# Performance work log

Measured on AMD Instinct MI355X. Metric: run time of the kernel, lower is better.

Reference implementation:

```python
import jax, jax.numpy as jnp
import numpy as np

N_NODES = 100000
N_EDGES = 1000000
IN_DIM = 64
HID = 64
OUT_DIM = 32
NUM_GRAPHS = 512


def setup_inputs() -> dict:
    key = jax.random.key(0)
    ks = jax.random.split(key, 16)
    x = jax.random.normal(ks[0], (N_NODES, IN_DIM), dtype=jnp.float32)
    edge_index = jax.random.randint(ks[1], (2, N_EDGES), 0, N_NODES, dtype=jnp.int64)
    batch = jnp.sort(jax.random.randint(ks[2], (N_NODES,), 0, NUM_GRAPHS, dtype=jnp.int64))

    def lin(k, i, o):
        s = 1.0 / np.sqrt(i)
        kw, kb = jax.random.split(k)
        return (jax.random.uniform(kw, (i, o), jnp.float32, -s, s),
                jax.random.uniform(kb, (o,), jnp.float32, -s, s))

    W1a, b1a = lin(ks[3], IN_DIM, HID)
    W2a, b2a = lin(ks[4], HID, HID)
    W1b, b1b = lin(ks[5], HID, HID)
    W2b, b2b = lin(ks[6], HID, HID)
    Wp1, bp1 = lin(ks[7], HID, HID)
    Wp2, bp2 = lin(ks[8], HID, OUT_DIM)
    return dict(x=x, edge_index=edge_index, batch=batch,
                W1a=W1a, b1a=b1a, W2a=W2a, b2a=b2a,
                W1b=W1b, b1b=b1b, W2b=W2b, b2b=b2b,
                Wp1=Wp1, bp1=bp1, Wp2=Wp2, bp2=bp2)


def _gin_layer(x, edge_index, W1, b1, W2, b2):
    # GINConv (eps=0): h_i = MLP(x_i + sum_{j->i} x_j)
    src, dst = edge_index[0], edge_index[1]
    agg = jax.ops.segment_sum(x[src], dst, num_segments=N_NODES)  # [N, d]
    h = x + agg
    h = jnp.maximum(h @ W1 + b1, 0.0) @ W2 + b2
    return h


def reference(x, edge_index, batch,
              W1a, b1a, W2a, b2a,
              W1b, b1b, W2b, b2b,
              Wp1, bp1, Wp2, bp2):
    # layer 0 (dropout is identity in eval mode)
    x = _gin_layer(x, edge_index, W1a, b1a, W2a, b2a)
    x = jnp.maximum(x, 0.0)
    # layer 1
    x = _gin_layer(x, edge_index, W1b, b1b, W2b, b2b)
    emb = x  # pre-ReLU embedding of last executed conv
    x = jnp.maximum(x, 0.0)
    # global mean pool over graphs
    sums = jax.ops.segment_sum(x, batch, num_segments=NUM_GRAPHS)  # [G, d]
    cnts = jax.ops.segment_sum(jnp.ones((x.shape[0],), x.dtype), batch, num_segments=NUM_GRAPHS)
    pooled = sums / jnp.maximum(cnts, 1.0)[:, None]
    # post-MLP (dropout identity in eval)
    out = (pooled @ Wp1 + bp1) @ Wp2 + bp2
    return emb, jax.nn.log_softmax(out, axis=1)
```

## Files before the change

kernel.cpp:

```cpp
#include <hip/hip_runtime.h>
#include <math.h>

#define N_NODES 100000
#define N_EDGES 1000000
#define HID 64
#define OUT_DIM 32
#define NUM_GRAPHS 512
#define CAP 48
#define NBUCK 98
#define BCAP 11264
#define ACHUNK 4096

typedef __attribute__((ext_vector_type(4))) float f4v;
typedef __attribute__((ext_vector_type(4))) int i4v;
typedef __attribute__((ext_vector_type(8))) short s8v;

static __device__ inline short f2bf(float f) {
  unsigned u = __float_as_uint(f);
  unsigned r = (u + 0x7fffu + ((u >> 16) & 1u)) >> 16;
  return (short)r;
}
static __device__ inline float bf2f(short s) {
  return __uint_as_float(((unsigned)(unsigned short)s) << 16);
}

__global__ __launch_bounds__(256) void prep_kernel(
    const float* __restrict__ W1a, const float* __restrict__ W2a,
    const float* __restrict__ W1b, const float* __restrict__ W2b,
    short* __restrict__ wtab, const int* __restrict__ batch,
    int* __restrict__ starts, int* __restrict__ bcnt) {
  int t = blockIdx.x * 256 + threadIdx.x;
  if (t < 16384) {
    int which = t >> 12;
    int r = t & 4095;
    const float* W = (which == 0) ? W1a : (which == 1) ? W2a : (which == 2) ? W1b : W2b;
    short* hiT = wtab + which * 8192;
    short* loT = hiT + 4096;
    int n = r & 63, k = r >> 6;
    float w = W[k * HID + n];
    short h = f2bf(w);
    hiT[n * HID + k] = h;
    loT[n * HID + k] = f2bf(w - bf2f(h));
  } else if (t < 16384 + NUM_GRAPHS + 1) {
    int g = t - 16384;
    int lo = 0, hi = N_NODES;
    while (lo < hi) {
      int mid = (lo + hi) >> 1;
      if (batch[mid] < g) lo = mid + 1; else hi = mid;
    }
    starts[g] = lo;
  } else if (t < 16384 + NUM_GRAPHS + 1 + NBUCK) {
    bcnt[t - 16384 - NUM_GRAPHS - 1] = 0;
  }
}

__global__ __launch_bounds__(256) void bucket_kernel(
    const int* __restrict__ ei, int* __restrict__ bedge,
    int* __restrict__ bcnt, int n_edges) {
  __shared__ int s_pack[ACHUNK];
  __shared__ unsigned char s_b[ACHUNK];
  __shared__ int s_sorted[ACHUNK];
  __shared__ int s_hist[NBUCK];
  __shared__ int s_off[NBUCK];
  __shared__ int s_base[NBUCK];

  int e0 = blockIdx.x * ACHUNK;
  int n = n_edges - e0;
  if (n > ACHUNK) n = ACHUNK;

  for (int i = threadIdx.x; i < NBUCK; i += 256) s_hist[i] = 0;
  __syncthreads();

  for (int i = threadIdx.x; i < n; i += 256) {
    int src = ei[e0 + i];
    int dst = ei[n_edges + e0 + i];
    int b = dst >> 10;
    s_pack[i] = src | ((dst & 1023) << 17);
    s_b[i] = (unsigned char)b;
    atomicAdd(&s_hist[b], 1);
  }
  __syncthreads();

  if (threadIdx.x == 0) {
    int run = 0;
    for (int b = 0; b < NBUCK; b++) { s_off[b] = run; run += s_hist[b]; }
  }
  if (threadIdx.x < NBUCK) {
    int c = s_hist[threadIdx.x];
    s_base[threadIdx.x] = c > 0 ? atomicAdd(&bcnt[threadIdx.x], c) : 0;
  }
  __syncthreads();

  for (int i = threadIdx.x; i < n; i += 256) {
    int p = atomicAdd(&s_off[s_b[i]], 1);
    s_sorted[p] = s_pack[i];
  }
  __syncthreads();

  int wv = threadIdx.x >> 6;
  int lane = threadIdx.x & 63;
  for (int b = wv; b < NBUCK; b += 4) {
    int cnt = s_hist[b];
    if (cnt == 0) continue;
    int start = s_off[b] - cnt;
    int gbase = s_base[b];
    for (int i = lane; i < cnt; i += 64) {
      int idx = gbase + i;
      if (idx < BCAP) bedge[b * BCAP + idx] = s_sorted[start + i];
    }
  }
}

__global__ __launch_bounds__(256) void csr_from_buckets_kernel(
    const int* __restrict__ bedge, const int* __restrict__ bcnt,
    int* __restrict__ deg, int* __restrict__ csr) {
  __shared__ int ldeg[1024];
  int b = blockIdx.x;
  int tid = threadIdx.x;
  for (int i = tid; i < 1024; i += 256) ldeg[i] = 0;
  __syncthreads();

  int n = bcnt[b];
  if (n > BCAP) n = BCAP;
  const int* bb = bedge + b * BCAP;
  for (int i0 = tid * 4; i0 < n; i0 += 1024) {
    int e0, e1, e2, e3;
    int rem = n - i0;
    if (rem >= 4) {
      i4v v = *(const i4v*)(bb + i0);
      e0 = v.x; e1 = v.y; e2 = v.z; e3 = v.w;
    } else {
      e0 = bb[i0];
      e1 = (rem > 1) ? bb[i0 + 1] : 0;
      e2 = (rem > 2) ? bb[i0 + 2] : 0;
      e3 = 0;
    }
    {
      int local = e0 >> 17, src = e0 & 0x1FFFF;
      int slot = atomicAdd(&ldeg[local], 1);
      if (slot < CAP) csr[(((size_t)b << 10) | local) * CAP + slot] = src;
    }
    if (n - i0 > 1) {
      int local = e1 >> 17, src = e1 & 0x1FFFF;
      int slot = atomicAdd(&ldeg[local], 1);
      if (slot < CAP) csr[(((size_t)b << 10) | local) * CAP + slot] = src;
    }
    if (n - i0 > 2) {
      int local = e2 >> 17, src = e2 & 0x1FFFF;
      int slot = atomicAdd(&ldeg[local], 1);
      if (slot < CAP) csr[(((size_t)b << 10) | local) * CAP + slot] = src;
    }
    if (n - i0 > 3) {
      int local = e3 >> 17, src = e3 & 0x1FFFF;
      int slot = atomicAdd(&ldeg[local], 1);
      if (slot < CAP) csr[(((size_t)b << 10) | local) * CAP + slot] = src;
    }
  }
  __syncthreads();

  for (int i = tid; i < 1024; i += 256) {
    int node = (b << 10) + i;
    if (node < N_NODES) deg[node] = ldeg[i];
  }
}

__global__ __launch_bounds__(256) void gather_kernel(
    const float* __restrict__ x, const int* __restrict__ deg,
    const int* __restrict__ csr, float* __restrict__ hbuf, int n_nodes) {
  int lane = threadIdx.x & 63;
  int node = blockIdx.x * (blockDim.x >> 6) + (threadIdx.x >> 6);
  if (node >= n_nodes) return;
  int g = lane >> 4;
  int sub = lane & 15;

  int idx = (lane < CAP) ? csr[node * CAP + lane] : 0;
  int d = deg[node];
  if (d > CAP) d = CAP;

  const f4v* x4 = (const f4v*)x;
  f4v a0 = (g == 0) ? x4[(size_t)node * 16 + sub] : (f4v){0.f, 0.f, 0.f, 0.f};
  f4v a1 = {0.f, 0.f, 0.f, 0.f};
  f4v a2 = {0.f, 0.f, 0.f, 0.f};
  f4v a3 = {0.f, 0.f, 0.f, 0.f};
  for (int j0 = 0; j0 < d; j0 += 16) {
    int j1 = j0 + g;
    int j2 = j0 + 4 + g;
    int j3 = j0 + 8 + g;
    int j4 = j0 + 12 + g;
    int s1 = __shfl(idx, j1);
    int s2 = __shfl(idx, j2);
    int s3 = __shfl(idx, j3);
    int s4 = __shfl(idx, j4);
    if (j1 < d) a0 += x4[(size_t)s1 * 16 + sub];
    if (j2 < d) a1 += x4[(size_t)s2 * 16 + sub];
    if (j3 < d) a2 += x4[(size_t)s3 * 16 + sub];
    if (j4 < d) a3 += x4[(size_t)s4 * 16 + sub];
  }
  f4v a = (a0 + a1) + (a2 + a3);
  a.x += __shfl_xor(a.x, 16); a.y += __shfl_xor(a.y, 16);
  a.z += __shfl_xor(a.z, 16); a.w += __shfl_xor(a.w, 16);
  a.x += __shfl_xor(a.x, 32); a.y += __shfl_xor(a.y, 32);
  a.z += __shfl_xor(a.z, 32); a.w += __shfl_xor(a.w, 32);
  if (g == 0) ((f4v*)hbuf)[(size_t)node * 16 + sub] = a;
}

#define LPAD 72

__global__ __launch_bounds__(256) void gin_mlp_mfma_kernel(
    const float* __restrict__ hbuf,
    const short* __restrict__ W1hi, const short* __restrict__ W1lo,
    const float* __restrict__ b1,
    const short* __restrict__ W2hi, const short* __restrict__ W2lo,
    const float* __restrict__ b2,
    float* __restrict__ out, int n_nodes, int apply_relu) {
  __shared__ short lds[4][2][16 * LPAD];

  int lane = threadIdx.x & 63;
  int wv = threadIdx.x >> 6;
  int m = lane & 15;
  int quad = lane >> 4;
  int nodeBase = blockIdx.x * 64 + wv * 16;
  int node = nodeBase + m;
  bool valid = node < n_nodes;

  s8v ahi[2], alo[2];
  for (int kb = 0; kb < 2; kb++) {
    int ks = kb * 32 + quad * 8;
    f4v r0 = {0.f, 0.f, 0.f, 0.f}, r1 = {0.f, 0.f, 0.f, 0.f};
    if (valid) {
      const f4v* hp = (const f4v*)(hbuf + (size_t)node * HID + ks);
      r0 = hp[0];
      r1 = hp[1];
    }
    s8v h, l;
#pragma unroll
    for (int j = 0; j < 8; j++) {
      float v = (j < 4) ? r0[j] : r1[j - 4];
      short hb = f2bf(v);
      h[j] = hb;
      l[j] = f2bf(v - bf2f(hb));
    }
    ahi[kb] = h;
    alo[kb] = l;
  }

  f4v acc[4];
#pragma unroll
  for (int nt = 0; nt < 4; nt++) acc[nt] = (f4v){0.f, 0.f, 0.f, 0.f};
#pragma unroll
  for (int kb = 0; kb < 2; kb++) {
#pragma unroll
    for (int nt = 0; nt < 4; nt++) {
      int n = nt * 16 + m;
      s8v bh = *(const s8v*)(W1hi + n * HID + kb * 32 + quad * 8);
      s8v bl = *(const s8v*)(W1lo + n * HID + kb * 32 + quad * 8);
      acc[nt] = __builtin_amdgcn_mfma_f32_16x16x32_bf16(ahi[kb], bh, acc[nt], 0, 0, 0);
      acc[nt] = __builtin_amdgcn_mfma_f32_16x16x32_bf16(ahi[kb], bl, acc[nt], 0, 0, 0);
      acc[nt] = __builtin_amdgcn_mfma_f32_16x16x32_bf16(alo[kb], bh, acc[nt], 0, 0, 0);
      acc[nt] = __builtin_amdgcn_mfma_f32_16x16x32_bf16(alo[kb], bl, acc[nt], 0, 0, 0);
    }
  }

  short* Lhi = lds[wv][0];
  short* Llo = lds[wv][1];
#pragma unroll
  for (int nt = 0; nt < 4; nt++) {
    int col = nt * 16 + m;
    float bb = b1[col];
#pragma unroll
    for (int r = 0; r < 4; r++) {
      int row = quad * 4 + r;
      float h = fmaxf(acc[nt][r] + bb, 0.f);
      short hb = f2bf(h);
      Lhi[row * LPAD + col] = hb;
      Llo[row * LPAD + col] = f2bf(h - bf2f(hb));
    }
  }
  __syncthreads();

  s8v a2hi[2], a2lo[2];
#pragma unroll
  for (int kb = 0; kb < 2; kb++) {
    int off = m * LPAD + kb * 32 + quad * 8;
    a2hi[kb] = *(const s8v*)(Lhi + off);
    a2lo[kb] = *(const s8v*)(Llo + off);
  }

  f4v acc2[4];
#pragma unroll
  for (int nt = 0; nt < 4; nt++) acc2[nt] = (f4v){0.f, 0.f, 0.f, 0.f};
#pragma unroll
  for (int kb = 0; kb < 2; kb++) {
#pragma unroll
    for (int nt = 0; nt < 4; nt++) {
      int n = nt * 16 + m;
      s8v bh = *(const s8v*)(W2hi + n * HID + kb * 32 + quad * 8);
      s8v bl = *(const s8v*)(W2lo + n * HID + kb * 32 + quad * 8);
      acc2[nt] = __builtin_amdgcn_mfma_f32_16x16x32_bf16(a2hi[kb], bh, acc2[nt], 0, 0, 0);
      acc2[nt] = __builtin_amdgcn_mfma_f32_16x16x32_bf16(a2hi[kb], bl, acc2[nt], 0, 0, 0);
      acc2[nt] = __builtin_amdgcn_mfma_f32_16x16x32_bf16(a2lo[kb], bh, acc2[nt], 0, 0, 0);
      acc2[nt] = __builtin_amdgcn_mfma_f32_16x16x32_bf16(a2lo[kb], bl, acc2[nt], 0, 0, 0);
    }
  }

#pragma unroll
  for (int nt = 0; nt < 4; nt++) {
    int col = nt * 16 + m;
    float bb = b2[col];
#pragma unroll
    for (int r = 0; r < 4; r++) {
      int row = quad * 4 + r;
      int onode = nodeBase + row;
      if (onode < n_nodes) {
        float o = acc2[nt][r] + bb;
        if (apply_relu) o = fmaxf(o, 0.f);
        out[(size_t)onode * HID + col] = o;
      }
    }
  }
}

__global__ __launch_bounds__(256) void poolhead_kernel(
    const float* __restrict__ emb, const int* __restrict__ starts,
    const float* __restrict__ Wp1, const float* __restrict__ bp1,
    const float* __restrict__ Wp2, const float* __restrict__ bp2,
    float* __restrict__ out) {
  int lane = threadIdx.x & 63;
  int g = blockIdx.x * 4 + (threadIdx.x >> 6);
  int group = lane >> 4, sub = lane & 15;
  int s0 = starts[g], s1 = starts[g + 1];

  const f4v* e4 = (const f4v*)emb;
  f4v acc = {0.f, 0.f, 0.f, 0.f};
  for (int n = s0 + group; n < s1; n += 4) {
    f4v v = e4[(size_t)n * 16 + sub];
    v.x = fmaxf(v.x, 0.f); v.y = fmaxf(v.y, 0.f);
    v.z = fmaxf(v.z, 0.f); v.w = fmaxf(v.w, 0.f);
    acc += v;
  }
  acc.x += __shfl_xor(acc.x, 16); acc.y += __shfl_xor(acc.y, 16);
  acc.z += __shfl_xor(acc.z, 16); acc.w += __shfl_xor(acc.w, 16);
  acc.x += __shfl_xor(acc.x, 32); acc.y += __shfl_xor(acc.y, 32);
  acc.z += __shfl_xor(acc.z, 32); acc.w += __shfl_xor(acc.w, 32);
  int srcl = lane >> 2;
  float v0 = __shfl(acc.x, srcl);
  float v1 = __shfl(acc.y, srcl);
  float v2 = __shfl(acc.z, srcl);
  float v3 = __shfl(acc.w, srcl);
  int r = lane & 3;
  float psum = (r == 0) ? v0 : (r == 1) ? v1 : (r == 2) ? v2 : v3;

  float c = fmaxf((float)(s1 - s0), 1.0f);
  float p = psum / c;

  float t = bp1[lane];
#pragma unroll
  for (int k = 0; k < HID; k++) {
    t += __shfl(p, k) * Wp1[k * HID + lane];
  }

  float acc2 = 0.0f;
#pragma unroll
  for (int k = 0; k < HID; k++) {
    float tk = __shfl(t, k);
    if (lane < OUT_DIM) acc2 += tk * Wp2[k * OUT_DIM + lane];
  }
  float o = (lane < OUT_DIM) ? (acc2 + bp2[lane]) : -1e30f;

  float m = o;
#pragma unroll
  for (int off = 32; off >= 1; off >>= 1) m = fmaxf(m, __shfl_xor(m, off));
  float ex = (lane < OUT_DIM) ? expf(o - m) : 0.0f;
  float s = ex;
#pragma unroll
  for (int off = 32; off >= 1; off >>= 1) s += __shfl_xor(s, off);
  float lse = m + logf(s);
  if (lane < OUT_DIM) out[g * OUT_DIM + lane] = o - lse;
}

extern "C" void kernel_launch(void* const* d_in, const int* in_sizes, int n_in,
                              void* d_out, int out_size, void* d_ws, size_t ws_size,
                              hipStream_t stream) {
  const float* x   = (const float*)d_in[0];
  const int* ei    = (const int*)d_in[1];
  const int* batch = (const int*)d_in[2];
  const float* W1a = (const float*)d_in[3];
  const float* b1a = (const float*)d_in[4];
  const float* W2a = (const float*)d_in[5];
  const float* b2a = (const float*)d_in[6];
  const float* W1b = (const float*)d_in[7];
  const float* b1b = (const float*)d_in[8];
  const float* W2b = (const float*)d_in[9];
  const float* b2b = (const float*)d_in[10];
  const float* Wp1 = (const float*)d_in[11];
  const float* bp1 = (const float*)d_in[12];
  const float* Wp2 = (const float*)d_in[13];
  const float* bp2 = (const float*)d_in[14];

  float* emb    = (float*)d_out;
  float* logits = (float*)d_out + (size_t)N_NODES * HID;
  float* x1 = emb;

  float* hbuf  = (float*)d_ws;
  int* bedge   = (int*)d_ws;
  int* bcnt    = bedge + NBUCK * BCAP;
  int* deg     = (int*)(hbuf + (size_t)N_NODES * HID);
  int* csr     = deg + N_NODES;
  int* starts  = csr + (size_t)N_NODES * CAP;
  short* wtab  = (short*)(starts + NUM_GRAPHS + 1);
  short* W1aHi = wtab + 0 * 4096; short* W1aLo = wtab + 1 * 4096;
  short* W2aHi = wtab + 2 * 4096; short* W2aLo = wtab + 3 * 4096;
  short* W1bHi = wtab + 4 * 4096; short* W1bLo = wtab + 5 * 4096;
  short* W2bHi = wtab + 6 * 4096; short* W2bLo = wtab + 7 * 4096;

  int prep_threads = 16384 + (NUM_GRAPHS + 1) + NBUCK;
  prep_kernel<<<(prep_threads + 255) / 256, 256, 0, stream>>>(
      W1a, W2a, W1b, W2b, wtab, batch, starts, bcnt);

  bucket_kernel<<<(N_EDGES + ACHUNK - 1) / ACHUNK, 256, 0, stream>>>(
      ei, bedge, bcnt, N_EDGES);
  csr_from_buckets_kernel<<<NBUCK, 256, 0, stream>>>(bedge, bcnt, deg, csr);

  int gather_blocks = (N_NODES + 3) / 4;
  int mlp_blocks = (N_NODES + 63) / 64;

  gather_kernel<<<gather_blocks, 256, 0, stream>>>(x, deg, csr, hbuf, N_NODES);
  gin_mlp_mfma_kernel<<<mlp_blocks, 256, 0, stream>>>(
      hbuf, W1aHi, W1aLo, b1a, W2aHi, W2aLo, b2a, x1, N_NODES, 1);

  gather_kernel<<<gather_blocks, 256, 0, stream>>>(x1, deg, csr, hbuf, N_NODES);
  gin_mlp_mfma_kernel<<<mlp_blocks, 256, 0, stream>>>(
      hbuf, W1bHi, W1bLo, b1b, W2bHi, W2bLo, b2b, emb, N_NODES, 0);

  poolhead_kernel<<<NUM_GRAPHS / 4, 256, 0, stream>>>(
      emb, starts, Wp1, bp1, Wp2, bp2, logits);
}
```

Baseline: 324.3 us.

## Split hi/lo bf16 in gather and parallelize bucket prefix scan

The fp32-to-bf16 hi/lo split moves from the MLP kernel into the gather epilogue, so the MLP kernel loads the split halves directly. The intermediate buffer keeps the same byte count but the conversion work now sits next to the reduction. The gather also loads only the first 16 CSR indices up front and fetches the rest only for nodes with degree above 16, which cuts index traffic for typical degree-10 nodes. The bucket kernel replaces its serial single-thread prefix sum with a parallel Hillis-Steele scan, at the cost of more barriers.

```diff
diff --git a/kernel.cpp b/kernel.cpp
--- a/kernel.cpp
+++ b/kernel.cpp
@@ -14,6 +14,7 @@
 typedef __attribute__((ext_vector_type(4))) float f4v;
 typedef __attribute__((ext_vector_type(4))) int i4v;
 typedef __attribute__((ext_vector_type(8))) short s8v;
+typedef __attribute__((ext_vector_type(4))) short s4vs;
 
 static __device__ inline short f2bf(float f) {
   unsigned u = __float_as_uint(f);
@@ -67,11 +68,12 @@
   int e0 = blockIdx.x * ACHUNK;
   int n = n_edges - e0;
   if (n > ACHUNK) n = ACHUNK;
-
-  for (int i = threadIdx.x; i < NBUCK; i += 256) s_hist[i] = 0;
-  __syncthreads();
-
-  for (int i = threadIdx.x; i < n; i += 256) {
+  int tid = threadIdx.x;
+
+  for (int i = tid; i < NBUCK; i += 256) s_hist[i] = 0;
+  __syncthreads();
+
+  for (int i = tid; i < n; i += 256) {
     int src = ei[e0 + i];
     int dst = ei[n_edges + e0 + i];
     int b = dst >> 10;
@@ -81,24 +83,31 @@
   }
   __syncthreads();
 
-  if (threadIdx.x == 0) {
-    int run = 0;
-    for (int b = 0; b < NBUCK; b++) { s_off[b] = run; run += s_hist[b]; }
-  }
-  if (threadIdx.x < NBUCK) {
-    int c = s_hist[threadIdx.x];
-    s_base[threadIdx.x] = c > 0 ? atomicAdd(&bcnt[threadIdx.x], c) : 0;
-  }
-  __syncthreads();
-
-  for (int i = threadIdx.x; i < n; i += 256) {
+  if (tid < NBUCK) s_off[tid] = s_hist[tid];
+  __syncthreads();
+  for (int off = 1; off < NBUCK; off <<= 1) {
+    int v = 0;
+    if (tid < NBUCK && tid >= off) v = s_off[tid - off];
+    __syncthreads();
+    if (tid < NBUCK && tid >= off) s_off[tid] += v;
+    __syncthreads();
+  }
+  if (tid < NBUCK) {
+    int excl = s_off[tid] - s_hist[tid];
+    s_off[tid] = excl;
+    int c = s_hist[tid];
+    s_base[tid] = c > 0 ? atomicAdd(&bcnt[tid], c) : 0;
+  }
+  __syncthreads();
+
+  for (int i = tid; i < n; i += 256) {
     int p = atomicAdd(&s_off[s_b[i]], 1);
     s_sorted[p] = s_pack[i];
   }
   __syncthreads();
 
-  int wv = threadIdx.x >> 6;
-  int lane = threadIdx.x & 63;
+  int wv = tid >> 6;
+  int lane = tid & 63;
   for (int b = wv; b < NBUCK; b += 4) {
     int cnt = s_hist[b];
     if (cnt == 0) continue;
@@ -166,27 +175,25 @@
 
 __global__ __launch_bounds__(256) void gather_kernel(
     const float* __restrict__ x, const int* __restrict__ deg,
-    const int* __restrict__ csr, float* __restrict__ hbuf, int n_nodes) {
+    const int* __restrict__ csr, short* __restrict__ hbufHi,
+    short* __restrict__ hbufLo, int n_nodes) {
   int lane = threadIdx.x & 63;
   int node = blockIdx.x * (blockDim.x >> 6) + (threadIdx.x >> 6);
   if (node >= n_nodes) return;
   int g = lane >> 4;
   int sub = lane & 15;
 
-  int idx = (lane < CAP) ? csr[node * CAP + lane] : 0;
+  const f4v* x4 = (const f4v*)x;
+  f4v a0 = (g == 0) ? x4[(size_t)node * 16 + sub] : (f4v){0.f, 0.f, 0.f, 0.f};
+  int idx = (lane < 16) ? csr[node * CAP + lane] : 0;
   int d = deg[node];
   if (d > CAP) d = CAP;
 
-  const f4v* x4 = (const f4v*)x;
-  f4v a0 = (g == 0) ? x4[(size_t)node * 16 + sub] : (f4v){0.f, 0.f, 0.f, 0.f};
   f4v a1 = {0.f, 0.f, 0.f, 0.f};
   f4v a2 = {0.f, 0.f, 0.f, 0.f};
   f4v a3 = {0.f, 0.f, 0.f, 0.f};
-  for (int j0 = 0; j0 < d; j0 += 16) {
-    int j1 = j0 + g;
-    int j2 = j0 + 4 + g;
-    int j3 = j0 + 8 + g;
-    int j4 = j0 + 12 + g;
+  if (d > 0) {
+    int j1 = g, j2 = 4 + g, j3 = 8 + g, j4 = 12 + g;
     int s1 = __shfl(idx, j1);
     int s2 = __shfl(idx, j2);
     int s3 = __shfl(idx, j3);
@@ -196,18 +203,43 @@
     if (j3 < d) a2 += x4[(size_t)s3 * 16 + sub];
     if (j4 < d) a3 += x4[(size_t)s4 * 16 + sub];
   }
+  if (d > 16) {
+    int idx2 = (lane < 32) ? csr[node * CAP + 16 + lane] : 0;
+    for (int j0 = 16; j0 < d; j0 += 16) {
+      int j1 = j0 + g, j2 = j0 + 4 + g, j3 = j0 + 8 + g, j4 = j0 + 12 + g;
+      int s1 = __shfl(idx2, j1 - 16);
+      int s2 = __shfl(idx2, j2 - 16);
+      int s3 = __shfl(idx2, j3 - 16);
+      int s4 = __shfl(idx2, j4 - 16);
+      if (j1 < d) a0 += x4[(size_t)s1 * 16 + sub];
+      if (j2 < d) a1 += x4[(size_t)s2 * 16 + sub];
+      if (j3 < d) a2 += x4[(size_t)s3 * 16 + sub];
+      if (j4 < d) a3 += x4[(size_t)s4 * 16 + sub];
+    }
+  }
   f4v a = (a0 + a1) + (a2 + a3);
   a.x += __shfl_xor(a.x, 16); a.y += __shfl_xor(a.y, 16);
   a.z += __shfl_xor(a.z, 16); a.w += __shfl_xor(a.w, 16);
   a.x += __shfl_xor(a.x, 32); a.y += __shfl_xor(a.y, 32);
   a.z += __shfl_xor(a.z, 32); a.w += __shfl_xor(a.w, 32);
-  if (g == 0) ((f4v*)hbuf)[(size_t)node * 16 + sub] = a;
+  if (g == 0) {
+    s4vs hi, lo;
+#pragma unroll
+    for (int c = 0; c < 4; c++) {
+      float v = a[c];
+      short hb = f2bf(v);
+      hi[c] = hb;
+      lo[c] = f2bf(v - bf2f(hb));
+    }
+    ((s4vs*)hbufHi)[(size_t)node * 16 + sub] = hi;
+    ((s4vs*)hbufLo)[(size_t)node * 16 + sub] = lo;
+  }
 }
 
 #define LPAD 72
 
 __global__ __launch_bounds__(256) void gin_mlp_mfma_kernel(
-    const float* __restrict__ hbuf,
+    const short* __restrict__ hbufHi, const short* __restrict__ hbufLo,
     const short* __restrict__ W1hi, const short* __restrict__ W1lo,
     const float* __restrict__ b1,
     const short* __restrict__ W2hi, const short* __restrict__ W2lo,
@@ -224,24 +256,16 @@
   bool valid = node < n_nodes;
 
   s8v ahi[2], alo[2];
+#pragma unroll
   for (int kb = 0; kb < 2; kb++) {
-    int ks = kb * 32 + quad * 8;
-    f4v r0 = {0.f, 0.f, 0.f, 0.f}, r1 = {0.f, 0.f, 0.f, 0.f};
+    int off = node * HID + kb * 32 + quad * 8;
     if (valid) {
-      const f4v* hp = (const f4v*)(hbuf + (size_t)node * HID + ks);
-      r0 = hp[0];
-      r1 = hp[1];
-    }
-    s8v h, l;
-#pragma unroll
-    for (int j = 0; j < 8; j++) {
-      float v = (j < 4) ? r0[j] : r1[j - 4];
-      short hb = f2bf(v);
-      h[j] = hb;
-      l[j] = f2bf(v - bf2f(hb));
-    }
-    ahi[kb] = h;
-    alo[kb] = l;
+      ahi[kb] = *(const s8v*)(hbufHi + off);
+      alo[kb] = *(const s8v*)(hbufLo + off);
+    } else {
+      ahi[kb] = (s8v){0, 0, 0, 0, 0, 0, 0, 0};
+      alo[kb] = (s8v){0, 0, 0, 0, 0, 0, 0, 0};
+    }
   }
 
   f4v acc[4];
@@ -401,10 +425,11 @@
   float* logits = (float*)d_out + (size_t)N_NODES * HID;
   float* x1 = emb;
 
-  float* hbuf  = (float*)d_ws;
+  short* hbufHi = (short*)d_ws;
+  short* hbufLo = hbufHi + (size_t)N_NODES * HID;
   int* bedge   = (int*)d_ws;
   int* bcnt    = bedge + NBUCK * BCAP;
-  int* deg     = (int*)(hbuf + (size_t)N_NODES * HID);
+  int* deg     = (int*)((float*)d_ws + (size_t)N_NODES * HID);
   int* csr     = deg + N_NODES;
   int* starts  = csr + (size_t)N_NODES * CAP;
   short* wtab  = (short*)(starts + NUM_GRAPHS + 1);
@@ -424,13 +449,15 @@
   int gather_blocks = (N_NODES + 3) / 4;
   int mlp_blocks = (N_NODES + 63) / 64;
 
-  gather_kernel<<<gather_blocks, 256, 0, stream>>>(x, deg, csr, hbuf, N_NODES);
+  gather_kernel<<<gather_blocks, 256, 0, stream>>>(
+      x, deg, csr, hbufHi, hbufLo, N_NODES);
   gin_mlp_mfma_kernel<<<mlp_blocks, 256, 0, stream>>>(
-      hbuf, W1aHi, W1aLo, b1a, W2aHi, W2aLo, b2a, x1, N_NODES, 1);
-
-  gather_kernel<<<gather_blocks, 256, 0, stream>>>(x1, deg, csr, hbuf, N_NODES);
+      hbufHi, hbufLo, W1aHi, W1aLo, b1a, W2aHi, W2aLo, b2a, x1, N_NODES, 1);
+
+  gather_kernel<<<gather_blocks, 256, 0, stream>>>(
+      x1, deg, csr, hbufHi, hbufLo, N_NODES);
   gin_mlp_mfma_kernel<<<mlp_blocks, 256, 0, stream>>>(
-      hbuf, W1bHi, W1bLo, b1b, W2bHi, W2bLo, b2b, emb, N_NODES, 0);
+      hbufHi, hbufLo, W1bHi, W1bLo, b1b, W2bHi, W2bLo, b2b, emb, N_NODES, 0);
 
   poolhead_kernel<<<NUM_GRAPHS / 4, 256, 0, stream>>>(
       emb, starts, Wp1, bp1, Wp2, bp2, logits);
```

Measured after the change: 322.7 us. About the same (-0.5%).
